# Kernel tuning notes

Measured on AMD Instinct MI355X. Metric: run time of the kernel, lower is better.

Reference implementation:

```python
import jax, jax.numpy as jnp
import numpy as np

NUM_COMPONENTS = 8
STRIDE, PADDING, OUTPUT_PADDING, K = 2, 1, 0, 4


def get_comp_mat(n):
    # Cayley-Dickson construction: entry [i, j] = +/- component index of the
    # weight multiplying input component j to produce output component i.
    A = np.array([[0]])
    while A.shape[0] < n:
        m = A.shape[0]
        A = np.vstack([np.hstack([A, -(A + m)]), np.hstack([A + m, A])])
    return A


def setup_inputs() -> dict:
    key = jax.random.key(0)
    k1, k2, k3 = jax.random.split(key, 3)
    B, Cin, Cout, H = 8, 512, 256, 64
    c_in, c_out = Cin // NUM_COMPONENTS, Cout // NUM_COMPONENTS
    x = jax.random.normal(k1, (B, Cin, H, H), jnp.float32)
    # per-component ConvTranspose2d weights, torch layout [C_in, C_out, kH, kW]
    W = jax.random.normal(k2, (NUM_COMPONENTS, c_in, c_out, K, K), jnp.float32) * 0.05
    b = jax.random.normal(k3, (NUM_COMPONENTS, c_out), jnp.float32) * 0.05
    return {"x": x, "W": W, "b": b}


def reference(x, W, b):
    n = NUM_COMPONENTS
    comp = get_comp_mat(n)                 # static [n, n] signed component table
    signs = jnp.asarray(np.where(comp < 0, -1.0, 1.0), x.dtype)
    idx = np.abs(comp)                     # which sub-conv weight to use
    c_in, c_out, kh, kw = W.shape[1:]
    # Fuse the n^2 transpose convs into ONE block transpose conv:
    # Kbig[j*c_in:(j+1)*c_in, i*c_out:(i+1)*c_out] = sign[i,j] * W[idx[i,j]]
    Wsel = W[idx] * signs[:, :, None, None, None, None]          # [ni, nj, c_in, c_out, kh, kw]
    Wbig = jnp.transpose(Wsel, (1, 2, 0, 3, 4, 5)).reshape(n * c_in, n * c_out, kh, kw)
    bbig = jnp.einsum('ij,ijc->ic', signs, b[idx]).reshape(n * c_out)
    # torch ConvTranspose2d == conv with input dilated by stride and flipped kernel
    rhs = jnp.flip(Wbig, (2, 3)).transpose(1, 0, 2, 3)           # OIHW
    pad = K - 1 - PADDING
    out = jax.lax.conv_general_dilated(
        x, rhs, window_strides=(1, 1),
        padding=((pad, pad + OUTPUT_PADDING), (pad, pad + OUTPUT_PADDING)),
        lhs_dilation=(STRIDE, STRIDE),
        dimension_numbers=('NCHW', 'OIHW', 'NCHW'))
    return out + bbig[None, :, None, None]
```

## Files before the change

### kernel.cpp

```cpp
#include <hip/hip_runtime.h>
#include <hip/hip_bf16.h>

typedef unsigned short ushort_t;
typedef __attribute__((ext_vector_type(8))) short short8;
typedef __attribute__((ext_vector_type(4))) float f32x4;

#define NCOMP    8
#define CIN      512
#define COUT     256
#define H        64
#define HP       66
#define OHW      128
#define NB       8

__device__ const int d_idx8[8][8] = {
    {0,1,2,1,4,3,2,3},
    {1,0,3,2,5,4,1,2},
    {2,1,0,1,6,5,4,3},
    {3,2,1,0,7,6,5,4},
    {4,3,2,3,0,1,2,1},
    {5,4,1,2,1,0,3,2},
    {6,5,4,3,2,1,0,1},
    {7,6,5,4,3,2,1,0}};

__device__ const int kh_tab[2][2] = {{1,3},{0,2}};
__device__ const int dh_tab[2][2] = {{0,-1},{1,0}};

__global__ void zero_halo(ushort_t* __restrict__ xpadT) {
    const int t = blockIdx.x * 256 + threadIdx.x;
    const int nA = 8 * 2 * 66 * 64;
    short8 z = {0, 0, 0, 0, 0, 0, 0, 0};
    if (t < nA) {
        int v  = t & 63;
        int r  = t >> 6;
        int iw = r % 66;
        int q  = r / 66;
        int ih = (q & 1) * 65;
        int b  = q >> 1;
        *(short8*)(xpadT + (((size_t)b * HP + ih) * HP + iw) * CIN + v * 8) = z;
    } else {
        int u  = t - nA;
        int v  = u & 63;
        int r  = u >> 6;
        int e  = r & 1;
        int q  = r >> 1;
        int ih = (q & 63) + 1;
        int b  = q >> 6;
        int iw = e * 65;
        *(short8*)(xpadT + (((size_t)b * HP + ih) * HP + iw) * CIN + v * 8) = z;
    }
}

__global__ void prep_x(const float* __restrict__ x, ushort_t* __restrict__ xpadT) {
    __shared__ ushort_t tile[32][33];
    const int ih  = blockIdx.x;
    const int iw0 = (blockIdx.y & 1) * 32;
    const int ic0 = (blockIdx.y >> 1) * 32;
    const int b   = blockIdx.z;
    const int t   = threadIdx.x;

    for (int e = t; e < 1024; e += 256) {
        int icl = e >> 5, iwl = e & 31;
        float v = x[(((size_t)b * CIN + ic0 + icl) * H + ih) * H + iw0 + iwl];
        __hip_bfloat16 h = __float2bfloat16(v);
        tile[icl][iwl] = *(ushort_t*)&h;
    }
    __syncthreads();
    const int iwl = t >> 3, g = t & 7;
    ushort4 v;
    v.x = tile[g * 4 + 0][iwl];
    v.y = tile[g * 4 + 1][iwl];
    v.z = tile[g * 4 + 2][iwl];
    v.w = tile[g * 4 + 3][iwl];
    ushort_t* dst = xpadT + (((size_t)b * HP + ih + 1) * HP + iw0 + iwl + 1) * CIN + ic0 + g * 4;
    *(ushort4*)dst = v;
}

__global__ void prep_w(const float* __restrict__ W, const float* __restrict__ bias,
                       ushort_t* __restrict__ Abf, float* __restrict__ bbig) {
    const int t = blockIdx.x * blockDim.x + threadIdx.x;
    if (t < 4 * 64 * 256 * 32) {
        int kin = t & 31;
        int oc  = (t >> 5) & 255;
        int ks  = (t >> 13) & 63;
        int cls = t >> 19;
        int k  = ks * 32 + kin;
        int a  = k >> 10, c = (k >> 9) & 1, ic = k & 511;
        int ph = cls >> 1, pw = cls & 1;
        int kh = kh_tab[ph][a], kw = kh_tab[pw][c];
        int i = oc >> 5, co = oc & 31;
        int j = ic >> 6, ci = ic & 63;
        float s = (i >= j) ? 1.0f : -1.0f;
        float v = s * W[(((size_t)(d_idx8[i][j] * 64 + ci) * 32 + co) * 4 + kh) * 4 + kw];
        __hip_bfloat16 h = __float2bfloat16(v);
        Abf[t] = *(ushort_t*)&h;
    }
    if (t < COUT) {
        int i = t >> 5, co = t & 31;
        float acc = 0.0f;
        for (int j = 0; j < NCOMP; ++j)
            acc += ((i >= j) ? 1.0f : -1.0f) * bias[d_idx8[i][j] * 32 + co];
        bbig[t] = acc;
    }
}

__device__ __forceinline__ void async16(void* lds_dst, const void* g_src) {
    __builtin_amdgcn_global_load_lds(
        (const __attribute__((address_space(1))) unsigned int*)g_src,
        (__attribute__((address_space(3))) unsigned int*)lds_dst,
        16, 0, 0);
}

#define STAGE(NS, CB)                                                          \
  {                                                                            \
    const int ns_  = (NS);                                                     \
    const int na_  = ns_ >> 5;                                                 \
    const int ncb_ = (ns_ >> 4) & 1;                                           \
    const int go_  = ((na_ ? dh1 : dh0) * HP + (ncb_ ? dw1 : dw0)) * CIN       \
                     + (ns_ & 15) * 32;                                        \
    const ushort_t* nap_ = Abf_t + (size_t)ns_ * 8192;                         \
    async16(sb + (CB) + t * 16,         nap_);                                 \
    async16(sb + (CB) + 8192 + t * 16,  nap_ + 4096);                          \
    async16(sb + (CB) + 16384 + t * 16, base_lo + go_);                        \
    async16(sb + (CB) + 24576 + t * 16, base_hi + go_);                        \
  }

#define COMPUTE(CB)                                                            \
  {                                                                            \
    short8 af[8], bf[4];                                                       \
    _Pragma("unroll")                                                          \
    for (int s = 0; s < 8; ++s)                                                \
      af[s] = *(const short8*)(sb + (CB) + aoff + s * 1024);                   \
    _Pragma("unroll")                                                          \
    for (int s = 0; s < 4; ++s)                                                \
      bf[s] = *(const short8*)(sb + (CB) + boff + s * 1024);                   \
    _Pragma("unroll")                                                          \
    for (int sm = 0; sm < 8; ++sm)                                             \
      _Pragma("unroll")                                                        \
      for (int sn = 0; sn < 4; ++sn)                                           \
        acc[sm][sn] = __builtin_amdgcn_mfma_f32_16x16x32_bf16(                 \
            af[sm], bf[sn], acc[sm][sn], 0, 0, 0);                             \
  }

#define WAITBAR(N)                                                             \
  asm volatile("s_waitcnt vmcnt(" #N ")" ::: "memory");                        \
  __builtin_amdgcn_s_barrier();                                                \
  __builtin_amdgcn_sched_barrier(0);

__launch_bounds__(512, 2)
__global__ void htconv_mfma(const ushort_t* __restrict__ xpadT,
                            const ushort_t* __restrict__ Abf,
                            const float* __restrict__ bbig,
                            float* __restrict__ out) {
    __shared__ __align__(16) ushort_t smem[65536];
    char* sb = (char*)smem;

    const int t     = threadIdx.x;
    const int ntile = blockIdx.x;
    const int cls   = blockIdx.z & 3;
    const int b     = blockIdx.z >> 2;
    const int ph = cls >> 1, pw = cls & 1;
    const int ohh0 = ntile * 4;

    const int srcc = (((t & 3) ^ ((t >> 3) & 3)) * 8);
    const ushort_t* Abf_t =
        Abf + ((size_t)cls * 64) * 8192 + ((size_t)(t >> 2)) * 32 + srcc;

    const int dh0 = dh_tab[ph][0], dh1 = dh_tab[ph][1];
    const int dw0 = dh_tab[pw][0], dw1 = dh_tab[pw][1];
    const int oww = (t >> 2) & 63;
    const int rlo = t >> 8;
    const ushort_t* base_lo =
        xpadT + (((size_t)b * HP + ohh0 + rlo + 1) * HP + oww + 1) * CIN + srcc;
    const ushort_t* base_hi = base_lo + (size_t)2 * HP * CIN;

    const int lane = t & 63, wave = t >> 6;
    const int wm = wave >> 2, wn = wave & 3;
    const int col = lane & 15, quad = lane >> 4;
    const int soff = (quad ^ ((col >> 1) & 3)) * 16;
    const int aoff = (wm * 128 + col) * 64 + soff;
    const int boff = 16384 + (wn * 64 + col) * 64 + soff;

    f32x4 acc[8][4];
#pragma unroll
    for (int i = 0; i < 8; ++i)
#pragma unroll
        for (int j = 0; j < 4; ++j)
            acc[i][j] = (f32x4){0.f, 0.f, 0.f, 0.f};

    STAGE(0, 0);
    STAGE(1, 32768);
    STAGE(2, 65536);

#pragma unroll 1
    for (int i = 0; i < 15; ++i) {
        const int n = 4 * i;
        WAITBAR(8); STAGE(n + 3, 98304); COMPUTE(0);
        WAITBAR(8); STAGE(n + 4, 0);     COMPUTE(32768);
        WAITBAR(8); STAGE(n + 5, 32768); COMPUTE(65536);
        WAITBAR(8); STAGE(n + 6, 65536); COMPUTE(98304);
    }
    WAITBAR(8); STAGE(63, 98304); COMPUTE(0);
    WAITBAR(8);                   COMPUTE(32768);
    WAITBAR(4);                   COMPUTE(65536);
    WAITBAR(0);                   COMPUTE(98304);

    const int oh = 2 * (ohh0 + wn) + ph;
#pragma unroll
    for (int sm = 0; sm < 8; ++sm) {
#pragma unroll
        for (int r = 0; r < 4; ++r) {
            const int occ = wm * 128 + sm * 16 + quad * 4 + r;
            const float bv = bbig[occ];
            float* obase = out + (((size_t)b * COUT + occ) * OHW + oh) * OHW + pw;
#pragma unroll
            for (int sn = 0; sn < 4; ++sn) {
                const int owi = sn * 16 + col;
                obase[2 * owi] = acc[sm][sn][r] + bv;
            }
        }
    }
}

extern "C" void kernel_launch(void* const* d_in, const int* in_sizes, int n_in,
                              void* d_out, int out_size, void* d_ws, size_t ws_size,
                              hipStream_t stream) {
    const float* x    = (const float*)d_in[0];
    const float* W    = (const float*)d_in[1];
    const float* bias = (const float*)d_in[2];
    float* out = (float*)d_out;

    ushort_t* xpadT = (ushort_t*)d_ws;
    ushort_t* Abf   = xpadT + (size_t)NB * HP * HP * CIN;
    float*    bbig  = (float*)(Abf + (size_t)4 * 64 * 256 * 32);

    zero_halo<<<dim3(520), 256, 0, stream>>>(xpadT);
    prep_x<<<dim3(H, 32, NB), 256, 0, stream>>>(x, xpadT);
    prep_w<<<dim3((4 * 64 * 256 * 32) / 256), 256, 0, stream>>>(W, bias, Abf, bbig);
    htconv_mfma<<<dim3(16, 1, 32), 512, 0, stream>>>(xpadT, Abf, bbig, out);
}
```

Before: 313.0 us.

## Fuse halo zeroing into row-wise x transpose kernel and raise MFMA priority

Replaces the separate halo-zeroing and 32x32-tile transpose kernels with one kernel that handles a full input row (all 512 channels × 64 columns) per block. It uses float4 loads and a swizzled LDS layout, writes 16-byte bf16 vectors, and also zeroes the halo rows and columns. This removes one launch and gives wider, more coalesced writes. It also wraps the MFMA block in s_setprio so the compute wave gets scheduling priority. The trade-off is a 64 KB LDS allocation per block, which lowers occupancy of the prep kernel.

```diff
diff --git a/kernel.cpp b/kernel.cpp
--- a/kernel.cpp
+++ b/kernel.cpp
@@ -26,54 +26,59 @@
 __device__ const int kh_tab[2][2] = {{1,3},{0,2}};
 __device__ const int dh_tab[2][2] = {{0,-1},{1,0}};
 
-__global__ void zero_halo(ushort_t* __restrict__ xpadT) {
-    const int t = blockIdx.x * 256 + threadIdx.x;
-    const int nA = 8 * 2 * 66 * 64;
-    short8 z = {0, 0, 0, 0, 0, 0, 0, 0};
-    if (t < nA) {
-        int v  = t & 63;
-        int r  = t >> 6;
-        int iw = r % 66;
-        int q  = r / 66;
-        int ih = (q & 1) * 65;
-        int b  = q >> 1;
-        *(short8*)(xpadT + (((size_t)b * HP + ih) * HP + iw) * CIN + v * 8) = z;
-    } else {
-        int u  = t - nA;
-        int v  = u & 63;
-        int r  = u >> 6;
-        int e  = r & 1;
-        int q  = r >> 1;
-        int ih = (q & 63) + 1;
-        int b  = q >> 6;
-        int iw = e * 65;
-        *(short8*)(xpadT + (((size_t)b * HP + ih) * HP + iw) * CIN + v * 8) = z;
-    }
-}
-
-__global__ void prep_x(const float* __restrict__ x, ushort_t* __restrict__ xpadT) {
-    __shared__ ushort_t tile[32][33];
-    const int ih  = blockIdx.x;
-    const int iw0 = (blockIdx.y & 1) * 32;
-    const int ic0 = (blockIdx.y >> 1) * 32;
-    const int b   = blockIdx.z;
-    const int t   = threadIdx.x;
-
-    for (int e = t; e < 1024; e += 256) {
-        int icl = e >> 5, iwl = e & 31;
-        float v = x[(((size_t)b * CIN + ic0 + icl) * H + ih) * H + iw0 + iwl];
-        __hip_bfloat16 h = __float2bfloat16(v);
-        tile[icl][iwl] = *(ushort_t*)&h;
+__global__ void prep_x2(const float* __restrict__ x, ushort_t* __restrict__ xpadT) {
+    __shared__ __align__(16) ushort_t lds[64 * 512];
+    const int t = threadIdx.x;
+    const int b = blockIdx.y;
+    const int ihb = blockIdx.x;
+
+    if (ihb == 64) {
+        short8 z = {0,0,0,0,0,0,0,0};
+        ushort_t* r0 = xpadT + ((size_t)b * HP + 0)  * HP * CIN;
+        ushort_t* r1 = xpadT + ((size_t)b * HP + 65) * HP * CIN;
+        for (int e = t; e < (HP * CIN) / 8; e += 256) {
+            *(short8*)(r0 + e * 8) = z;
+            *(short8*)(r1 + e * 8) = z;
+        }
+        return;
+    }
+    const int ih = ihb;
+
+    const int iv      = t & 15;
+    const int ic_base = t >> 4;
+    const float* xr = x + ((size_t)b * CIN * H + ih) * H;
+#pragma unroll 8
+    for (int r = 0; r < 32; ++r) {
+        const int ic = r * 16 + ic_base;
+        const float4 v = *(const float4*)(xr + (size_t)ic * H * H + iv * 4);
+        const int swz_ic = ic ^ (iv << 3);
+        __hip_bfloat16 h0 = __float2bfloat16(v.x);
+        __hip_bfloat16 h1 = __float2bfloat16(v.y);
+        __hip_bfloat16 h2 = __float2bfloat16(v.z);
+        __hip_bfloat16 h3 = __float2bfloat16(v.w);
+        lds[(iv * 4 + 0) * 512 + swz_ic] = *(ushort_t*)&h0;
+        lds[(iv * 4 + 1) * 512 + swz_ic] = *(ushort_t*)&h1;
+        lds[(iv * 4 + 2) * 512 + swz_ic] = *(ushort_t*)&h2;
+        lds[(iv * 4 + 3) * 512 + swz_ic] = *(ushort_t*)&h3;
     }
     __syncthreads();
-    const int iwl = t >> 3, g = t & 7;
-    ushort4 v;
-    v.x = tile[g * 4 + 0][iwl];
-    v.y = tile[g * 4 + 1][iwl];
-    v.z = tile[g * 4 + 2][iwl];
-    v.w = tile[g * 4 + 3][iwl];
-    ushort_t* dst = xpadT + (((size_t)b * HP + ih + 1) * HP + iw0 + iwl + 1) * CIN + ic0 + g * 4;
-    *(ushort4*)dst = v;
+
+    ushort_t* rowc = xpadT + (((size_t)b * HP + ih + 1) * HP) * CIN;
+    ushort_t* dst  = rowc + CIN;
+#pragma unroll
+    for (int r = 0; r < 16; ++r) {
+        const int e   = r * 256 + t;
+        const int iw  = e >> 6;
+        const int ic0 = (e & 63) * 8;
+        const int off = iw * 512 + (ic0 ^ ((iw >> 2) << 3));
+        *(short8*)(dst + (size_t)e * 8) = *(const short8*)(lds + off);
+    }
+    if (t < 128) {
+        short8 z = {0,0,0,0,0,0,0,0};
+        const int l = t & 63;
+        ushort_t* hc = (t < 64) ? rowc : (rowc + 65 * CIN);
+        *(short8*)(hc + l * 8) = z;
+    }
 }
 
 __global__ void prep_w(const float* __restrict__ W, const float* __restrict__ bias,
@@ -134,12 +139,14 @@
     _Pragma("unroll")                                                          \
     for (int s = 0; s < 4; ++s)                                                \
       bf[s] = *(const short8*)(sb + (CB) + boff + s * 1024);                   \
+    __builtin_amdgcn_s_setprio(1);                                             \
     _Pragma("unroll")                                                          \
     for (int sm = 0; sm < 8; ++sm)                                             \
       _Pragma("unroll")                                                        \
       for (int sn = 0; sn < 4; ++sn)                                           \
         acc[sm][sn] = __builtin_amdgcn_mfma_f32_16x16x32_bf16(                 \
             af[sm], bf[sn], acc[sm][sn], 0, 0, 0);                             \
+    __builtin_amdgcn_s_setprio(0);                                             \
   }
 
 #define WAITBAR(N)                                                             \
@@ -234,8 +241,7 @@
     ushort_t* Abf   = xpadT + (size_t)NB * HP * HP * CIN;
     float*    bbig  = (float*)(Abf + (size_t)4 * 64 * 256 * 32);
 
-    zero_halo<<<dim3(520), 256, 0, stream>>>(xpadT);
-    prep_x<<<dim3(H, 32, NB), 256, 0, stream>>>(x, xpadT);
+    prep_x2<<<dim3(65, NB), 256, 0, stream>>>(x, xpadT);
     prep_w<<<dim3((4 * 64 * 256 * 32) / 256), 256, 0, stream>>>(W, bias, Abf, bbig);
     htconv_mfma<<<dim3(16, 1, 32), 512, 0, stream>>>(xpadT, Abf, bbig, out);
 }
```

Measured after the change: 307.9 us. Within noise of the previous version (-1.6%).
